# Performance work log

Hardware: AMD Instinct MI355X
Metric: run time of the kernel (lower is better)

Reference implementation:

```python
import jax, jax.numpy as jnp
import numpy as np

H, W = 4096, 4096
MIN_VAL, MAX_VAL = 0, 256
D = MAX_VAL - MIN_VAL - 1  # 255 candidate thresholds t = 0..254
N_BINS = MAX_VAL           # pixel values live in [0, 256)


def setup_inputs() -> dict:
    key = jax.random.key(0)
    img = jax.random.randint(key, (H, W), MIN_VAL, MAX_VAL, dtype=jnp.int32)
    return {"img_HxW": img}


def reference(img_HxW):
    hw = H * W
    flat = img_HxW.ravel()
    # Histogram of pixel counts and pixel-value sums (float32 accumulation,
    # matching torch.sum(..., dtype=torch.float32) in the original).
    cnt = jax.ops.segment_sum(jnp.ones_like(flat, jnp.float32), flat, num_segments=N_BINS)
    val_sum = jax.ops.segment_sum(flat.astype(jnp.float32), flat, num_segments=N_BINS)
    # Cumulative sums give, for each threshold t, the count/sum of pixels <= t.
    # This equals the original's broadcast compare + masked sum over [H*W, d].
    num_b = jnp.cumsum(cnt)[:D]        # pixels in class "black" (<= t)
    sum_b = jnp.cumsum(val_sum)[:D]    # sum of those pixels
    num_w = hw - num_b                  # pixels in class "white" (> t)
    sum_w = jnp.sum(val_sum) - sum_b
    mean_b = sum_b / num_b
    mean_w = sum_w / num_w
    var_hist = num_b * num_w * (mean_b - mean_w) ** 2  # inter-class variance
    thresh = jnp.argmax(var_hist).astype(jnp.int32)
    bin_img = jnp.where(img_HxW <= thresh,
                        jnp.int32(MIN_VAL), jnp.int32(MAX_VAL))
    return thresh, bin_img
```

## Files before the change

kernel.cpp:

```cpp
#include <hip/hip_runtime.h>

#define HW_TOTAL (4096 * 4096)
#define NBINS 256
#define NCHUNK (HW_TOTAL / 4)
#define NSUB 16

#define HGRID 256
#define HCPT 16

#define BGRID 512
#define BBATCH 8

#define BLK 1024

typedef int int4n __attribute__((ext_vector_type(4)));
typedef int int4a __attribute__((ext_vector_type(4), aligned(4)));

#define WS_NEED (HGRID * NBINS * 4 + 256)

template <int MODE>
__global__ __launch_bounds__(BLK, 8) void otsu_hist_k(const int4* __restrict__ img4,
                                                      unsigned* __restrict__ out) {
    __shared__ unsigned h[NSUB * NBINS];
    const int t = threadIdx.x;
    for (int i = t; i < NSUB * NBINS; i += BLK) h[i] = 0;
    __syncthreads();

    unsigned* hp = h + ((t & (NSUB - 1)) << 8);
    const int wave = t >> 6, lane = t & 63;
    const int i0 = blockIdx.x * (BLK * HCPT) + wave * (64 * HCPT) + lane;

#pragma unroll
    for (int half = 0; half < 2; ++half) {
        int4 v[8];
        const int j0 = i0 + half * (8 * 64);
#pragma unroll
        for (int k = 0; k < 8; ++k) v[k] = img4[j0 + k * 64];
#pragma unroll
        for (int k = 0; k < 8; ++k) {
            atomicAdd(&hp[(unsigned)v[k].x], 1u);
            atomicAdd(&hp[(unsigned)v[k].y], 1u);
            atomicAdd(&hp[(unsigned)v[k].z], 1u);
            atomicAdd(&hp[(unsigned)v[k].w], 1u);
        }
    }
    __syncthreads();

    if (t < NBINS) {
        unsigned s = 0;
#pragma unroll
        for (int ss = 0; ss < NSUB; ++ss) s += h[(ss << 8) | t];
        if (MODE == 0) {
            out[blockIdx.x * NBINS + t] = s;
        } else {
            if (s) atomicAdd(&out[t], s);
        }
    }
}

__global__ __launch_bounds__(1024) void otsu_thresh_k(const unsigned* __restrict__ partials,
                                                      int B,
                                                      int* __restrict__ d_out,
                                                      int* __restrict__ thresh_ws) {
    __shared__ unsigned red[4][NBINS];
    __shared__ unsigned cnt[NBINS];

    const int bin = threadIdx.x & 255;
    const int q = threadIdx.x >> 8;
    const int BQ = (B + 3) / 4;
    int r = q * BQ;
    const int e = min((q + 1) * BQ, B);
    unsigned s = 0;
    for (; r + 16 <= e; r += 16) {
#pragma unroll
        for (int k = 0; k < 16; ++k) s += partials[(r + k) * NBINS + bin];
    }
    for (; r < e; ++r) s += partials[r * NBINS + bin];
    red[q][bin] = s;
    __syncthreads();

    if (threadIdx.x < NBINS)
        cnt[bin] = red[0][bin] + red[1][bin] + red[2][bin] + red[3][bin];
    __syncthreads();

    if (threadIdx.x >= 64) return;
    const int lane = threadIdx.x;

    uint4 c4 = ((const uint4*)cnt)[lane];
    unsigned cs[4] = {c4.x, c4.y, c4.z, c4.w};

    unsigned long long lc[4], lv[4];
    unsigned long long ccum = 0ull, vcum = 0ull;
#pragma unroll
    for (int k = 0; k < 4; ++k) {
        ccum += cs[k];
        vcum += (unsigned long long)cs[k] * (unsigned)(4 * lane + k);
        lc[k] = ccum;
        lv[k] = vcum;
    }
    unsigned long long cscan = ccum, vscan = vcum;
    for (int d = 1; d < 64; d <<= 1) {
        unsigned long long cu = __shfl_up(cscan, d);
        unsigned long long vu = __shfl_up(vscan, d);
        if (lane >= d) { cscan += cu; vscan += vu; }
    }
    const unsigned long long cbase = cscan - ccum;
    const unsigned long long vbase = vscan - vcum;
    const unsigned long long vtotal = __shfl(vscan, 63);

    double best = -1.0;
    int bestt = 255;
    const double hw = (double)HW_TOTAL;
    const double vtot_d = (double)vtotal;
#pragma unroll
    for (int k = 0; k < 4; ++k) {
        int tt = 4 * lane + k;
        if (tt > 254) continue;
        double nb = (double)(cbase + lc[k]);
        double sb = (double)(vbase + lv[k]);
        double nw = hw - nb;
        double sw = vtot_d - sb;
        double dm = sb / nb - sw / nw;
        double var = nb * nw * dm * dm;
        if (var > best || (var == best && tt < bestt)) { best = var; bestt = tt; }
    }
    for (int d = 32; d >= 1; d >>= 1) {
        double ov = __shfl_xor(best, d);
        int ot = __shfl_xor(bestt, d);
        if (ov > best || (ov == best && ot < bestt)) { best = ov; bestt = ot; }
    }
    if (lane == 0) {
        d_out[0] = bestt;
        *thresh_ws = bestt;
    }
}

__global__ __launch_bounds__(BLK, 8) void otsu_bin_k(const int* __restrict__ img,
                                                     int* __restrict__ out,
                                                     const int* __restrict__ thresh_ws) {
    const int thresh = *thresh_ws;
    const int t = threadIdx.x;
    const int wave = t >> 6, lane = t & 63;
    const int i0 = blockIdx.x * (BLK * BBATCH) + wave * (64 * BBATCH) + lane;

#pragma unroll
    for (int k = 0; k < BBATCH; ++k) {
        const int c = i0 + k * 64;
        const int4a* vp = (const int4a*)(img + (c ? 4 * c - 1 : 0));
        int4a v = *vp;
        int4n o;
        o.x = (v.x <= thresh) ? 0 : 256;
        o.y = (v.y <= thresh) ? 0 : 256;
        o.z = (v.z <= thresh) ? 0 : 256;
        o.w = (v.w <= thresh) ? 0 : 256;
        if (c == 0) {
            o.w = o.z; o.z = o.y; o.y = o.x; o.x = thresh;
        }
        __builtin_nontemporal_store(o, (int4n*)out + c);
    }
    if (i0 == 0)
        out[HW_TOTAL] = (img[HW_TOTAL - 1] <= thresh) ? 0 : 256;
}

extern "C" void kernel_launch(void* const* d_in, const int* in_sizes, int n_in,
                              void* d_out, int out_size, void* d_ws, size_t ws_size,
                              hipStream_t stream) {
    const int* img = (const int*)d_in[0];
    int* out = (int*)d_out;
    int* thresh_ws = (int*)d_ws;
    unsigned* hist_buf = (unsigned*)((char*)d_ws + 256);

    if (ws_size >= (size_t)WS_NEED) {
        otsu_hist_k<0><<<HGRID, BLK, 0, stream>>>((const int4*)img, hist_buf);
        otsu_thresh_k<<<1, 1024, 0, stream>>>(hist_buf, HGRID, out, thresh_ws);
    } else {
        (void)hipMemsetAsync(hist_buf, 0, NBINS * sizeof(unsigned), stream);
        otsu_hist_k<1><<<HGRID, BLK, 0, stream>>>((const int4*)img, hist_buf);
        otsu_thresh_k<<<1, 1024, 0, stream>>>(hist_buf, 1, out, thresh_ws);
    }
    otsu_bin_k<<<BGRID, BLK, 0, stream>>>(img, out, thresh_ws);
}
```

Baseline: 42.38 us.

## Fuse threshold computation into binarize kernel, dropping the single-block launch

The single-block threshold kernel is removed. Every block of the binarize kernel now reduces the 256 per-block histogram partials itself, runs the Otsu scan in one wave, and shares the threshold through LDS. This removes one kernel launch and the serial gap of a one-block kernel between histogram and binarization. The cost is that each of the 512 blocks re-reads 256x256 partials (256 KB each, mostly L2 hits), which adds redundant traffic and latency before each block starts its streaming work.

```diff
diff --git a/kernel.cpp b/kernel.cpp
--- a/kernel.cpp
+++ b/kernel.cpp
@@ -18,74 +18,7 @@
 
 #define WS_NEED (HGRID * NBINS * 4 + 256)
 
-template <int MODE>
-__global__ __launch_bounds__(BLK, 8) void otsu_hist_k(const int4* __restrict__ img4,
-                                                      unsigned* __restrict__ out) {
-    __shared__ unsigned h[NSUB * NBINS];
-    const int t = threadIdx.x;
-    for (int i = t; i < NSUB * NBINS; i += BLK) h[i] = 0;
-    __syncthreads();
-
-    unsigned* hp = h + ((t & (NSUB - 1)) << 8);
-    const int wave = t >> 6, lane = t & 63;
-    const int i0 = blockIdx.x * (BLK * HCPT) + wave * (64 * HCPT) + lane;
-
-#pragma unroll
-    for (int half = 0; half < 2; ++half) {
-        int4 v[8];
-        const int j0 = i0 + half * (8 * 64);
-#pragma unroll
-        for (int k = 0; k < 8; ++k) v[k] = img4[j0 + k * 64];
-#pragma unroll
-        for (int k = 0; k < 8; ++k) {
-            atomicAdd(&hp[(unsigned)v[k].x], 1u);
-            atomicAdd(&hp[(unsigned)v[k].y], 1u);
-            atomicAdd(&hp[(unsigned)v[k].z], 1u);
-            atomicAdd(&hp[(unsigned)v[k].w], 1u);
-        }
-    }
-    __syncthreads();
-
-    if (t < NBINS) {
-        unsigned s = 0;
-#pragma unroll
-        for (int ss = 0; ss < NSUB; ++ss) s += h[(ss << 8) | t];
-        if (MODE == 0) {
-            out[blockIdx.x * NBINS + t] = s;
-        } else {
-            if (s) atomicAdd(&out[t], s);
-        }
-    }
-}
-
-__global__ __launch_bounds__(1024) void otsu_thresh_k(const unsigned* __restrict__ partials,
-                                                      int B,
-                                                      int* __restrict__ d_out,
-                                                      int* __restrict__ thresh_ws) {
-    __shared__ unsigned red[4][NBINS];
-    __shared__ unsigned cnt[NBINS];
-
-    const int bin = threadIdx.x & 255;
-    const int q = threadIdx.x >> 8;
-    const int BQ = (B + 3) / 4;
-    int r = q * BQ;
-    const int e = min((q + 1) * BQ, B);
-    unsigned s = 0;
-    for (; r + 16 <= e; r += 16) {
-#pragma unroll
-        for (int k = 0; k < 16; ++k) s += partials[(r + k) * NBINS + bin];
-    }
-    for (; r < e; ++r) s += partials[r * NBINS + bin];
-    red[q][bin] = s;
-    __syncthreads();
-
-    if (threadIdx.x < NBINS)
-        cnt[bin] = red[0][bin] + red[1][bin] + red[2][bin] + red[3][bin];
-    __syncthreads();
-
-    if (threadIdx.x >= 64) return;
-    const int lane = threadIdx.x;
-
+__device__ __forceinline__ int otsu_scan64(const unsigned* cnt, int lane) {
     uint4 c4 = ((const uint4*)cnt)[lane];
     unsigned cs[4] = {c4.x, c4.y, c4.z, c4.w};
 
@@ -129,33 +62,95 @@
         int ot = __shfl_xor(bestt, d);
         if (ov > best || (ov == best && ot < bestt)) { best = ov; bestt = ot; }
     }
-    if (lane == 0) {
-        d_out[0] = bestt;
-        *thresh_ws = bestt;
+    return bestt;
+}
+
+template <int MODE>
+__global__ __launch_bounds__(BLK, 8) void otsu_hist_k(const int4* __restrict__ img4,
+                                                      unsigned* __restrict__ out) {
+    __shared__ unsigned h[NSUB * NBINS];
+    const int t = threadIdx.x;
+    for (int i = t; i < NSUB * NBINS; i += BLK) h[i] = 0;
+    __syncthreads();
+
+    unsigned* hp = h + ((t & (NSUB - 1)) << 8);
+    const int wave = t >> 6, lane = t & 63;
+    const int i0 = blockIdx.x * (BLK * HCPT) + wave * (64 * HCPT) + lane;
+
+#pragma unroll
+    for (int half = 0; half < 2; ++half) {
+        int4 v[8];
+        const int j0 = i0 + half * (8 * 64);
+#pragma unroll
+        for (int k = 0; k < 8; ++k) v[k] = img4[j0 + k * 64];
+#pragma unroll
+        for (int k = 0; k < 8; ++k) {
+            atomicAdd(&hp[(unsigned)v[k].x], 1u);
+            atomicAdd(&hp[(unsigned)v[k].y], 1u);
+            atomicAdd(&hp[(unsigned)v[k].z], 1u);
+            atomicAdd(&hp[(unsigned)v[k].w], 1u);
+        }
+    }
+    __syncthreads();
+
+    if (t < NBINS) {
+        unsigned s = 0;
+#pragma unroll
+        for (int ss = 0; ss < NSUB; ++ss) s += h[(ss << 8) | t];
+        if (MODE == 0) {
+            out[blockIdx.x * NBINS + t] = s;
+        } else {
+            if (s) atomicAdd(&out[t], s);
+        }
     }
 }
 
 __global__ __launch_bounds__(BLK, 8) void otsu_bin_k(const int* __restrict__ img,
                                                      int* __restrict__ out,
-                                                     const int* __restrict__ thresh_ws) {
-    const int thresh = *thresh_ws;
+                                                     const unsigned* __restrict__ partials,
+                                                     int B) {
+    __shared__ unsigned red[4][NBINS];
+    __shared__ unsigned cnt[NBINS];
+    __shared__ int s_thresh;
+
     const int t = threadIdx.x;
+    const int bin = t & 255;
+    const int q = t >> 8;
+    const int BQ = (B + 3) / 4;
+    {
+        int r = q * BQ;
+        const int e = min((q + 1) * BQ, B);
+        unsigned s = 0;
+        for (; r + 16 <= e; r += 16) {
+#pragma unroll
+            for (int k = 0; k < 16; ++k) s += partials[(r + k) * NBINS + bin];
+        }
+        for (; r < e; ++r) s += partials[r * NBINS + bin];
+        red[q][bin] = s;
+    }
+    __syncthreads();
+    if (t < NBINS)
+        cnt[bin] = red[0][bin] + red[1][bin] + red[2][bin] + red[3][bin];
+    __syncthreads();
+    if (t < 64) {
+        int bt = otsu_scan64(cnt, t);
+        if (t == 0) s_thresh = bt;
+    }
+    __syncthreads();
+    const int thresh = s_thresh;
+
     const int wave = t >> 6, lane = t & 63;
     const int i0 = blockIdx.x * (BLK * BBATCH) + wave * (64 * BBATCH) + lane;
-
 #pragma unroll
     for (int k = 0; k < BBATCH; ++k) {
         const int c = i0 + k * 64;
-        const int4a* vp = (const int4a*)(img + (c ? 4 * c - 1 : 0));
-        int4a v = *vp;
+        int4a v = *(const int4a*)(img + (c ? 4 * c - 1 : 0));
         int4n o;
         o.x = (v.x <= thresh) ? 0 : 256;
         o.y = (v.y <= thresh) ? 0 : 256;
         o.z = (v.z <= thresh) ? 0 : 256;
         o.w = (v.w <= thresh) ? 0 : 256;
-        if (c == 0) {
-            o.w = o.z; o.z = o.y; o.y = o.x; o.x = thresh;
-        }
+        if (c == 0) { o.w = o.z; o.z = o.y; o.y = o.x; o.x = thresh; }
         __builtin_nontemporal_store(o, (int4n*)out + c);
     }
     if (i0 == 0)
@@ -167,16 +162,14 @@
                               hipStream_t stream) {
     const int* img = (const int*)d_in[0];
     int* out = (int*)d_out;
-    int* thresh_ws = (int*)d_ws;
     unsigned* hist_buf = (unsigned*)((char*)d_ws + 256);
 
     if (ws_size >= (size_t)WS_NEED) {
         otsu_hist_k<0><<<HGRID, BLK, 0, stream>>>((const int4*)img, hist_buf);
-        otsu_thresh_k<<<1, 1024, 0, stream>>>(hist_buf, HGRID, out, thresh_ws);
+        otsu_bin_k<<<BGRID, BLK, 0, stream>>>(img, out, hist_buf, HGRID);
     } else {
         (void)hipMemsetAsync(hist_buf, 0, NBINS * sizeof(unsigned), stream);
         otsu_hist_k<1><<<HGRID, BLK, 0, stream>>>((const int4*)img, hist_buf);
-        otsu_thresh_k<<<1, 1024, 0, stream>>>(hist_buf, 1, out, thresh_ws);
+        otsu_bin_k<<<BGRID, BLK, 0, stream>>>(img, out, hist_buf, 1);
     }
-    otsu_bin_k<<<BGRID, BLK, 0, stream>>>(img, out, thresh_ws);
 }
```

After: 41.96 us. No clear change (-1.0%).
